# Performance work log

Hardware: AMD Instinct MI355X
Metric: run time of the kernel (lower is better)

## Reference

```python
import jax, jax.numpy as jnp
import numpy as np

B, P = 32, 1024
HID, H, D = 512, 8, 64   # hidden_dim, heads, head_dim
MEM, RANK = 64, 64


def setup_inputs() -> dict:
    key = jax.random.key(0)
    ks = jax.random.split(key, 12)
    s1 = 1.0  # Linear(1, hidden): fan_in = 1 -> torch init bound = 1
    sh = 1.0 / np.sqrt(HID)
    sd = 1.0 / np.sqrt(D)
    return {
        "x":    jax.random.normal(ks[0], (B, P), dtype=jnp.float32),
        # q/k/v: Linear(1, hidden) -> weight (hidden,), bias (hidden,)
        "w_q": jax.random.uniform(ks[1], (HID,), jnp.float32, -s1, s1),
        "b_q": jax.random.uniform(ks[2], (HID,), jnp.float32, -s1, s1),
        "w_k": jax.random.uniform(ks[3], (HID,), jnp.float32, -s1, s1),
        "b_k": jax.random.uniform(ks[4], (HID,), jnp.float32, -s1, s1),
        "w_v": jax.random.uniform(ks[5], (HID,), jnp.float32, -s1, s1),
        "b_v": jax.random.uniform(ks[6], (HID,), jnp.float32, -s1, s1),
        # mem_proj: Linear(head_dim, mem_size, bias=False) -> weight (mem, d)
        "w_mem": jax.random.uniform(ks[7], (MEM, D), jnp.float32, -sd, sd),
        # project_to_U / V: Linear(hidden, rank)
        "w_u":  jax.random.uniform(ks[8], (RANK, HID), jnp.float32, -sh, sh),
        "b_u":  jax.random.uniform(ks[9], (RANK,), jnp.float32, -sh, sh),
        "w_v2": jax.random.uniform(ks[10], (RANK, HID), jnp.float32, -sh, sh),
        "b_v2": jax.random.uniform(ks[11], (RANK,), jnp.float32, -sh, sh),
    }


def reference(x, w_q, b_q, w_k, b_k, w_v, b_v, w_mem, w_u, b_u, w_v2, b_v2):
    Bx, p = x.shape
    xu = x[..., None]                                  # (B, p, 1)
    # Linear(1, hidden) is a scalar broadcast: x * w + b
    def to_heads(w, b):
        y = xu * w + b                                 # (B, p, HID)
        return y.reshape(Bx, p, H, D).transpose(0, 2, 1, 3)  # (B, H, p, D)
    Q = to_heads(w_q, b_q)
    K = to_heads(w_k, b_k)
    V = to_heads(w_v, b_v)

    phi = lambda u: jax.nn.elu(u) + 1.0
    Qf = phi(Q)                                        # (B, H, p, D)
    # memory weights: softmax over the p axis (dim=2)
    W_mem = jax.nn.softmax(jnp.einsum('bhpd,md->bhpm', K, w_mem), axis=2)
    mem_KV = jnp.einsum('bhpm,bhpd->bhmd', W_mem, V)   # (B, H, MEM, D)
    attn = jnp.einsum('bhpd,bhmd->bhpm', Qf, mem_KV)   # (B, H, p, MEM)
    h = jnp.einsum('bhpm,bhmd->bhpd', attn, mem_KV)    # (B, H, p, D)
    h = h.transpose(0, 2, 1, 3).reshape(Bx, p, H * D)  # (B, p, HID)

    U = h @ w_u.T + b_u                                # (B, p, RANK)
    Vp = h @ w_v2.T + b_v2                             # (B, p, RANK)
    coeffs_k = jnp.einsum('bpr,bqr->bpq', U, Vp)       # (B, p, p)
    return coeffs_k
```

## Files before the change

kernel.cpp:

```cpp
#include <hip/hip_runtime.h>
#include <hip/hip_bf16.h>

#define BB 32
#define PP 1024
#define HID 512
#define NH 8
#define DD 64
#define MEM 64
#define RANK 64

typedef float f32x4 __attribute__((ext_vector_type(4)));

#define A_OFF   0
#define M_OFF   512
#define T_OFF   1024
#define G_OFF   18432

__global__ __launch_bounds__(1024) void k_precompute(
    const float* __restrict__ wk, const float* __restrict__ wmem,
    const float* __restrict__ wv, const float* __restrict__ bv,
    const float* __restrict__ wu, const float* __restrict__ bu,
    const float* __restrict__ wv2, const float* __restrict__ bv2,
    float* __restrict__ A, float* __restrict__ M17) {
  __shared__ float WU[17 * 64];
  __shared__ float WVt[64 * 17];
  const int t = threadIdx.x;
  const int r = t >> 4;
  const int dq = t & 15;

  const float4 wm4 = *(const float4*)&wmem[r * DD + dq * 4];
  for (int h = 0; h < NH; ++h) {
    const float4 wk4 = *(const float4*)&wk[h * DD + dq * 4];
    float s = wm4.x * wk4.x + wm4.y * wk4.y + wm4.z * wk4.z + wm4.w * wk4.w;
    s += __shfl_xor(s, 1); s += __shfl_xor(s, 2);
    s += __shfl_xor(s, 4); s += __shfl_xor(s, 8);
    if (dq == 0) A[h * MEM + r] = s;
  }

  for (int j = 0; j < 17; ++j) {
    float su, sv;
    if (j < 16) {
      const int hh = j & 7;
      const float4 w4 = (j < 8) ? *(const float4*)&wv[hh * DD + dq * 4]
                                : *(const float4*)&bv[hh * DD + dq * 4];
      const float4 u4 = *(const float4*)&wu[r * HID + hh * DD + dq * 4];
      const float4 v4 = *(const float4*)&wv2[r * HID + hh * DD + dq * 4];
      su = u4.x * w4.x + u4.y * w4.y + u4.z * w4.z + u4.w * w4.w;
      sv = v4.x * w4.x + v4.y * w4.y + v4.z * w4.z + v4.w * w4.w;
    } else {
      su = (dq == 0) ? bu[r] : 0.f;
      sv = (dq == 0) ? bv2[r] : 0.f;
    }
    su += __shfl_xor(su, 1); su += __shfl_xor(su, 2);
    su += __shfl_xor(su, 4); su += __shfl_xor(su, 8);
    sv += __shfl_xor(sv, 1); sv += __shfl_xor(sv, 2);
    sv += __shfl_xor(sv, 4); sv += __shfl_xor(sv, 8);
    if (dq == 0) {
      WU[j * 64 + r] = su;
      WVt[r * 17 + j] = sv;
    }
  }
  __syncthreads();

  if (t < 17 * 17) {
    const int ii = t / 17, jj = t - ii * 17;
    float s = 0.f;
    for (int rr = 0; rr < 64; ++rr) s += WU[ii * 64 + rr] * WVt[rr * 17 + jj];
    M17[t] = s;
  }
}

__global__ __launch_bounds__(256) void k_memsoftmax(
    const float* __restrict__ x, const float* __restrict__ A,
    float* __restrict__ T) {
  const int wid = blockIdx.x * 4 + (threadIdx.x >> 6);
  const int lane = threadIdx.x & 63;
  const int b = wid >> 9;
  const int hm = wid & 511;
  const float a = A[hm];
  const float* xr = x + b * PP;

  float xs[16];
  float mx = -INFINITY;
#pragma unroll
  for (int k = 0; k < 16; ++k) {
    xs[k] = xr[lane + k * 64];
    mx = fmaxf(mx, xs[k] * a);
  }
#pragma unroll
  for (int off = 32; off >= 1; off >>= 1) mx = fmaxf(mx, __shfl_xor(mx, off));

  float s = 0.f, sx = 0.f;
#pragma unroll
  for (int k = 0; k < 16; ++k) {
    const float e = __expf(xs[k] * a - mx);
    s += e;
    sx += e * xs[k];
  }
#pragma unroll
  for (int off = 32; off >= 1; off >>= 1) {
    s += __shfl_xor(s, off);
    sx += __shfl_xor(sx, off);
  }
  if (lane == 0) T[wid] = sx / s;
}

__global__ __launch_bounds__(256) void k_features(
    const float* __restrict__ x, const float* __restrict__ wq,
    const float* __restrict__ bq, const float* __restrict__ wv,
    const float* __restrict__ bv, const float* __restrict__ T,
    float* __restrict__ G) {
  __shared__ float sS1, sS2;
  const int idx0 = blockIdx.x * 256;
  const int b = idx0 >> 13;
  const int h = (idx0 >> 10) & 7;
  const int p = (idx0 & 1023) + threadIdx.x;
  const int t = threadIdx.x;

  if (t < 64) {
    const float v = T[(b * NH + h) * MEM + t];
    float s1 = v, s2 = v * v;
#pragma unroll
    for (int off = 32; off >= 1; off >>= 1) {
      s1 += __shfl_xor(s1, off);
      s2 += __shfl_xor(s2, off);
    }
    if (t == 0) { sS1 = s1; sS2 = s2; }
  }

  const float xv = x[b * PP + p];
  float a1 = 0.f, a0 = 0.f;
#pragma unroll 8
  for (int d = 0; d < DD; ++d) {
    const float q = xv * wq[h * DD + d] + bq[h * DD + d];
    const float ph = (q > 0.f) ? (q + 1.f) : __expf(q);
    a1 += ph * wv[h * DD + d];
    a0 += ph * bv[h * DD + d];
  }
  __syncthreads();
  const float s1 = sS1, s2 = sS2;
  const float c1 = a1 * s2 + a0 * s1;
  const float c2 = a1 * s1 + a0 * (float)MEM;
  G[(b * 16 + h) * PP + p] = c1;
  G[(b * 16 + 8 + h) * PP + p] = c2;
}

__global__ __launch_bounds__(256) void k_coeffs(
    const float* __restrict__ G, const float* __restrict__ M17,
    float* __restrict__ out) {
  __shared__ float Ml[17 * 17];
  __shared__ float Gp[16 * 128];
  __shared__ float Gq[16 * 128];
  __shared__ float Fl[17 * 128];
  const int b = blockIdx.z;
  const int p0 = blockIdx.y * 128;
  const int q0 = blockIdx.x * 128;
  const int t = threadIdx.x;
  const float* Gg = G + (size_t)b * 16 * PP;

  for (int i = t; i < 17 * 17; i += 256) Ml[i] = M17[i];
  for (int i = t; i < 16 * 128; i += 256) {
    const int row = i >> 7, col = i & 127;
    Gp[i] = Gg[row * PP + p0 + col];
    Gq[i] = Gg[row * PP + q0 + col];
  }
  __syncthreads();

  for (int i = t; i < 17 * 128; i += 256) {
    const int j = i >> 7, pp = i & 127;
    float f = Ml[16 * 17 + j];
#pragma unroll
    for (int ii = 0; ii < 16; ++ii) f += Gp[ii * 128 + pp] * Ml[ii * 17 + j];
    Fl[i] = f;
  }
  __syncthreads();

  const int pr = t >> 4;
  const int qv = t & 15;

  float acc[8][8];
#pragma unroll
  for (int r = 0; r < 8; ++r) {
    const float f16 = Fl[16 * 128 + pr * 8 + r];
#pragma unroll
    for (int c = 0; c < 8; ++c) acc[r][c] = f16;
  }

#pragma unroll
  for (int j = 0; j < 16; ++j) {
    const float4 fj0 = *(const float4*)&Fl[j * 128 + pr * 8];
    const float4 fj1 = *(const float4*)&Fl[j * 128 + pr * 8 + 4];
    const float4 gj0 = *(const float4*)&Gq[j * 128 + qv * 8];
    const float4 gj1 = *(const float4*)&Gq[j * 128 + qv * 8 + 4];
    const float fr[8] = {fj0.x, fj0.y, fj0.z, fj0.w, fj1.x, fj1.y, fj1.z, fj1.w};
    const float gc[8] = {gj0.x, gj0.y, gj0.z, gj0.w, gj1.x, gj1.y, gj1.z, gj1.w};
#pragma unroll
    for (int r = 0; r < 8; ++r) {
#pragma unroll
      for (int c = 0; c < 8; ++c) acc[r][c] += fr[r] * gc[c];
    }
  }

  const size_t base = ((size_t)b * PP + p0 + pr * 8) * PP + q0 + qv * 8;
#pragma unroll
  for (int r = 0; r < 8; ++r) {
    const f32x4 v0 = {acc[r][0], acc[r][1], acc[r][2], acc[r][3]};
    const f32x4 v1 = {acc[r][4], acc[r][5], acc[r][6], acc[r][7]};
    __builtin_nontemporal_store(v0, (f32x4*)&out[base + (size_t)r * PP]);
    __builtin_nontemporal_store(v1, (f32x4*)&out[base + (size_t)r * PP + 4]);
  }
}

extern "C" void kernel_launch(void* const* d_in, const int* in_sizes, int n_in,
                              void* d_out, int out_size, void* d_ws, size_t ws_size,
                              hipStream_t stream) {
  const float* x    = (const float*)d_in[0];
  const float* wq   = (const float*)d_in[1];
  const float* bq   = (const float*)d_in[2];
  const float* wk   = (const float*)d_in[3];
  const float* bk   = (const float*)d_in[4];  (void)bk;
  const float* wv   = (const float*)d_in[5];
  const float* bv   = (const float*)d_in[6];
  const float* wmem = (const float*)d_in[7];
  const float* wu   = (const float*)d_in[8];
  const float* bu   = (const float*)d_in[9];
  const float* wv2  = (const float*)d_in[10];
  const float* bv2  = (const float*)d_in[11];

  float* ws = (float*)d_ws;
  float* A   = ws + A_OFF;
  float* M17 = ws + M_OFF;
  float* T   = ws + T_OFF;
  float* G   = ws + G_OFF;
  float* out = (float*)d_out;

  k_precompute<<<1, 1024, 0, stream>>>(wk, wmem, wv, bv, wu, bu, wv2, bv2, A, M17);
  k_memsoftmax<<<4096, 256, 0, stream>>>(x, A, T);
  k_features<<<1024, 256, 0, stream>>>(x, wq, bq, wv, bv, T, G);
  k_coeffs<<<dim3(8, 8, 32), 256, 0, stream>>>(G, M17, out);
}
```

Measured before the change: 217.3 us.

## Fuse precompute, memory softmax and feature kernels into one launch

Three kernels (weight precompute, per-(b,h,m) softmax statistics, per-position features) become one 1024-thread kernel: 256 blocks each handle one (batch, head), and an extra block computes the 17x17 rank matrix. The softmax scale A is recomputed in-block with a wave reduction, and T stays in shared memory instead of making a global round trip. This removes two kernel launches and the intermediate buffers, at the cost of only 257 large blocks for the front end and some redundant weight dot products.

```diff
diff --git a/kernel.cpp b/kernel.cpp
--- a/kernel.cpp
+++ b/kernel.cpp
@@ -11,114 +11,101 @@
 
 typedef float f32x4 __attribute__((ext_vector_type(4)));
 
-#define A_OFF   0
 #define M_OFF   512
-#define T_OFF   1024
 #define G_OFF   18432
 
-__global__ __launch_bounds__(1024) void k_precompute(
-    const float* __restrict__ wk, const float* __restrict__ wmem,
+__global__ __launch_bounds__(1024) void k_fused(
+    const float* __restrict__ x, const float* __restrict__ wq,
+    const float* __restrict__ bq, const float* __restrict__ wk,
     const float* __restrict__ wv, const float* __restrict__ bv,
-    const float* __restrict__ wu, const float* __restrict__ bu,
-    const float* __restrict__ wv2, const float* __restrict__ bv2,
-    float* __restrict__ A, float* __restrict__ M17) {
-  __shared__ float WU[17 * 64];
-  __shared__ float WVt[64 * 17];
+    const float* __restrict__ wmem, const float* __restrict__ wu,
+    const float* __restrict__ bu, const float* __restrict__ wv2,
+    const float* __restrict__ bv2, float* __restrict__ G,
+    float* __restrict__ M17) {
   const int t = threadIdx.x;
-  const int r = t >> 4;
-  const int dq = t & 15;
-
-  const float4 wm4 = *(const float4*)&wmem[r * DD + dq * 4];
-  for (int h = 0; h < NH; ++h) {
-    const float4 wk4 = *(const float4*)&wk[h * DD + dq * 4];
-    float s = wm4.x * wk4.x + wm4.y * wk4.y + wm4.z * wk4.z + wm4.w * wk4.w;
-    s += __shfl_xor(s, 1); s += __shfl_xor(s, 2);
-    s += __shfl_xor(s, 4); s += __shfl_xor(s, 8);
-    if (dq == 0) A[h * MEM + r] = s;
-  }
-
-  for (int j = 0; j < 17; ++j) {
-    float su, sv;
-    if (j < 16) {
-      const int hh = j & 7;
-      const float4 w4 = (j < 8) ? *(const float4*)&wv[hh * DD + dq * 4]
-                                : *(const float4*)&bv[hh * DD + dq * 4];
-      const float4 u4 = *(const float4*)&wu[r * HID + hh * DD + dq * 4];
-      const float4 v4 = *(const float4*)&wv2[r * HID + hh * DD + dq * 4];
-      su = u4.x * w4.x + u4.y * w4.y + u4.z * w4.z + u4.w * w4.w;
-      sv = v4.x * w4.x + v4.y * w4.y + v4.z * w4.z + v4.w * w4.w;
-    } else {
-      su = (dq == 0) ? bu[r] : 0.f;
-      sv = (dq == 0) ? bv2[r] : 0.f;
-    }
-    su += __shfl_xor(su, 1); su += __shfl_xor(su, 2);
-    su += __shfl_xor(su, 4); su += __shfl_xor(su, 8);
-    sv += __shfl_xor(sv, 1); sv += __shfl_xor(sv, 2);
-    sv += __shfl_xor(sv, 4); sv += __shfl_xor(sv, 8);
-    if (dq == 0) {
-      WU[j * 64 + r] = su;
-      WVt[r * 17 + j] = sv;
-    }
-  }
-  __syncthreads();
-
-  if (t < 17 * 17) {
-    const int ii = t / 17, jj = t - ii * 17;
-    float s = 0.f;
-    for (int rr = 0; rr < 64; ++rr) s += WU[ii * 64 + rr] * WVt[rr * 17 + jj];
-    M17[t] = s;
-  }
-}
-
-__global__ __launch_bounds__(256) void k_memsoftmax(
-    const float* __restrict__ x, const float* __restrict__ A,
-    float* __restrict__ T) {
-  const int wid = blockIdx.x * 4 + (threadIdx.x >> 6);
-  const int lane = threadIdx.x & 63;
-  const int b = wid >> 9;
-  const int hm = wid & 511;
-  const float a = A[hm];
+
+  if (blockIdx.x == 256) {
+    __shared__ float WU[17 * 64];
+    __shared__ float WVt[64 * 17];
+    const int r = t >> 4;
+    const int dq = t & 15;
+    for (int j = 0; j < 17; ++j) {
+      float su, sv;
+      if (j < 16) {
+        const int hh = j & 7;
+        const float4 w4 = (j < 8) ? *(const float4*)&wv[hh * DD + dq * 4]
+                                  : *(const float4*)&bv[hh * DD + dq * 4];
+        const float4 u4 = *(const float4*)&wu[r * HID + hh * DD + dq * 4];
+        const float4 v4 = *(const float4*)&wv2[r * HID + hh * DD + dq * 4];
+        su = u4.x * w4.x + u4.y * w4.y + u4.z * w4.z + u4.w * w4.w;
+        sv = v4.x * w4.x + v4.y * w4.y + v4.z * w4.z + v4.w * w4.w;
+      } else {
+        su = (dq == 0) ? bu[r] : 0.f;
+        sv = (dq == 0) ? bv2[r] : 0.f;
+      }
+      su += __shfl_xor(su, 1); su += __shfl_xor(su, 2);
+      su += __shfl_xor(su, 4); su += __shfl_xor(su, 8);
+      sv += __shfl_xor(sv, 1); sv += __shfl_xor(sv, 2);
+      sv += __shfl_xor(sv, 4); sv += __shfl_xor(sv, 8);
+      if (dq == 0) {
+        WU[j * 64 + r] = su;
+        WVt[r * 17 + j] = sv;
+      }
+    }
+    __syncthreads();
+    if (t < 17 * 17) {
+      const int ii = t / 17, jj = t - ii * 17;
+      float s = 0.f;
+      for (int rr = 0; rr < 64; ++rr) s += WU[ii * 64 + rr] * WVt[rr * 17 + jj];
+      M17[t] = s;
+    }
+    return;
+  }
+
+  __shared__ float Tl[MEM];
+  __shared__ float sS1, sS2;
+  const int b = blockIdx.x >> 3;
+  const int h = blockIdx.x & 7;
+  const int w = t >> 6;
+  const int lane = t & 63;
   const float* xr = x + b * PP;
 
+  const float xv = xr[t];
+
   float xs[16];
-  float mx = -INFINITY;
-#pragma unroll
-  for (int k = 0; k < 16; ++k) {
-    xs[k] = xr[lane + k * 64];
-    mx = fmaxf(mx, xs[k] * a);
-  }
-#pragma unroll
-  for (int off = 32; off >= 1; off >>= 1) mx = fmaxf(mx, __shfl_xor(mx, off));
-
-  float s = 0.f, sx = 0.f;
-#pragma unroll
-  for (int k = 0; k < 16; ++k) {
-    const float e = __expf(xs[k] * a - mx);
-    s += e;
-    sx += e * xs[k];
-  }
-#pragma unroll
-  for (int off = 32; off >= 1; off >>= 1) {
-    s += __shfl_xor(s, off);
-    sx += __shfl_xor(sx, off);
-  }
-  if (lane == 0) T[wid] = sx / s;
-}
-
-__global__ __launch_bounds__(256) void k_features(
-    const float* __restrict__ x, const float* __restrict__ wq,
-    const float* __restrict__ bq, const float* __restrict__ wv,
-    const float* __restrict__ bv, const float* __restrict__ T,
-    float* __restrict__ G) {
-  __shared__ float sS1, sS2;
-  const int idx0 = blockIdx.x * 256;
-  const int b = idx0 >> 13;
-  const int h = (idx0 >> 10) & 7;
-  const int p = (idx0 & 1023) + threadIdx.x;
-  const int t = threadIdx.x;
+#pragma unroll
+  for (int k = 0; k < 16; ++k) xs[k] = xr[lane + k * 64];
+
+  for (int mi = 0; mi < 4; ++mi) {
+    const int m = w * 4 + mi;
+    float a = wk[h * DD + lane] * wmem[m * DD + lane];
+#pragma unroll
+    for (int off = 32; off >= 1; off >>= 1) a += __shfl_xor(a, off);
+
+    float mx = -INFINITY;
+#pragma unroll
+    for (int k = 0; k < 16; ++k) mx = fmaxf(mx, xs[k] * a);
+#pragma unroll
+    for (int off = 32; off >= 1; off >>= 1) mx = fmaxf(mx, __shfl_xor(mx, off));
+
+    float s = 0.f, sx = 0.f;
+#pragma unroll
+    for (int k = 0; k < 16; ++k) {
+      const float e = __expf(xs[k] * a - mx);
+      s += e;
+      sx += e * xs[k];
+    }
+#pragma unroll
+    for (int off = 32; off >= 1; off >>= 1) {
+      s += __shfl_xor(s, off);
+      sx += __shfl_xor(sx, off);
+    }
+    if (lane == 0) Tl[m] = sx / s;
+  }
+  __syncthreads();
 
   if (t < 64) {
-    const float v = T[(b * NH + h) * MEM + t];
+    const float v = Tl[t];
     float s1 = v, s2 = v * v;
 #pragma unroll
     for (int off = 32; off >= 1; off >>= 1) {
@@ -127,8 +114,8 @@
     }
     if (t == 0) { sS1 = s1; sS2 = s2; }
   }
-
-  const float xv = x[b * PP + p];
+  __syncthreads();
+
   float a1 = 0.f, a0 = 0.f;
 #pragma unroll 8
   for (int d = 0; d < DD; ++d) {
@@ -137,12 +124,11 @@
     a1 += ph * wv[h * DD + d];
     a0 += ph * bv[h * DD + d];
   }
-  __syncthreads();
   const float s1 = sS1, s2 = sS2;
   const float c1 = a1 * s2 + a0 * s1;
   const float c2 = a1 * s1 + a0 * (float)MEM;
-  G[(b * 16 + h) * PP + p] = c1;
-  G[(b * 16 + 8 + h) * PP + p] = c2;
+  G[(b * 16 + h) * PP + t] = c1;
+  G[(b * 16 + 8 + h) * PP + t] = c2;
 }
 
 __global__ __launch_bounds__(256) void k_coeffs(
@@ -228,14 +214,11 @@
   const float* bv2  = (const float*)d_in[11];
 
   float* ws = (float*)d_ws;
-  float* A   = ws + A_OFF;
   float* M17 = ws + M_OFF;
-  float* T   = ws + T_OFF;
   float* G   = ws + G_OFF;
   float* out = (float*)d_out;
 
-  k_precompute<<<1, 1024, 0, stream>>>(wk, wmem, wv, bv, wu, bu, wv2, bv2, A, M17);
-  k_memsoftmax<<<4096, 256, 0, stream>>>(x, A, T);
-  k_features<<<1024, 256, 0, stream>>>(x, wq, bq, wv, bv, T, G);
+  k_fused<<<257, 1024, 0, stream>>>(x, wq, bq, wk, wv, bv, wmem, wu, bu,
+                                    wv2, bv2, G, M17);
   k_coeffs<<<dim3(8, 8, 32), 256, 0, stream>>>(G, M17, out);
 }
```

Result: faster. 210.7 us (-3.0%).
